# Kernel tuning notes

Measured on AMD Instinct MI355X. Metric: run time of the kernel, lower is better.

## Reference

```python
import jax, jax.numpy as jnp
import numpy as np

IN_CH, OUT_CH, M1, M2 = 64, 64, 32, 32


def _powerlaw_psd_gaussian(key, exponent, n):
    """JAX port of colorednoise.powerlaw_psd_gaussian (fmin=0 default)."""
    f = jnp.fft.rfftfreq(n).astype(jnp.float32)  # [n//2+1]
    # fmin = max(0, 1/n); f[0]=0 is the only freq below it -> clamp to f[1]
    s_scale = jnp.where(f < 1.0 / n, f[1], f) ** (-exponent / 2.0)
    w = s_scale[1:]
    w = w.at[-1].multiply((1 + (n % 2)) / 2.0)  # Nyquist correction
    sigma = 2.0 * jnp.sqrt(jnp.sum(w * w)) / n
    kr, ki = jax.random.split(key)
    sr = jax.random.normal(kr, f.shape, jnp.float32) * s_scale
    si = jax.random.normal(ki, f.shape, jnp.float32) * s_scale
    if n % 2 == 0:
        si = si.at[-1].set(0.0)
        sr = sr.at[-1].multiply(jnp.sqrt(2.0))
    si = si.at[0].set(0.0)
    sr = sr.at[0].multiply(jnp.sqrt(2.0))
    return jnp.fft.irfft(sr + 1j * si, n=n) / sigma


def _compl_mul2d(t1, w, e_r, e_i, amp_r, amp_i, phi_r, phi_i, key):
    # Faithful to the torch code: stack over in-ch at dim=1 then sum dim=2
    # sums over the OUT channel axis => out[b,i,x,y] = t1[b,i,x,y]*sum_o w[i,o,x,y]
    out = t1 * jnp.sum(w, axis=1)[None]  # [B, IN_CH, M1, M2] complex
    b, c, m1, m2 = out.shape
    n = b * c * m1 * m2
    k1, k2 = jax.random.split(key)
    nr = jnp.roll(_powerlaw_psd_gaussian(k1, e_r, n), phi_r.astype(jnp.int32)) * amp_r
    ni = jnp.roll(_powerlaw_psd_gaussian(k2, e_i, n), phi_i.astype(jnp.int32)) * amp_i
    # original multiplies imag noise by amp_i twice (once in-place, once on reshape)
    noise = (nr + 1j * (ni * amp_i)).reshape(b, c, m1, m2)
    return out - noise


def _forward(x, w1, w2, exp_r, exp_i, nAmp_real, nAmp_imag, nPhase_real, nphase_imag):
    w1c = w1[..., 0] + 1j * w1[..., 1]  # [IN, OUT, M1, M2] complex64
    w2c = w2[..., 0] + 1j * w2[..., 1]
    e_r = jnp.median(exp_r)
    e_i = jnp.median(exp_i)
    amp_r = jnp.median(nAmp_real)
    amp_i = jnp.median(nAmp_imag)
    phi_r = jnp.median(nPhase_real)
    phi_i = jnp.median(nphase_imag)
    B, _, H, W = x.shape
    Wr = W // 2 + 1
    x_ft = jnp.fft.rfft2(x)  # [B, IN_CH, H, Wr]
    key = jax.random.key(42)
    kA, kB = jax.random.split(key)
    out_ft = jnp.zeros((B, OUT_CH, H, Wr), jnp.complex64)
    out_ft = out_ft.at[:, :, :M1, :M2].set(
        _compl_mul2d(x_ft[:, :, :M1, :M2], w1c, e_r, e_i, amp_r, amp_i, phi_r, phi_i, kA))
    out_ft = out_ft.at[:, :, -M1:, :M2].set(
        _compl_mul2d(x_ft[:, :, -M1:, :M2], w2c, e_r, e_i, amp_r, amp_i, phi_r, phi_i, kB))
    return jnp.fft.irfft2(out_ft, s=(H, W)).astype(jnp.float32)


def setup_inputs() -> dict:
    key = jax.random.key(0)
    ks = jax.random.split(key, 9)
    scale = 1.0 / (IN_CH * OUT_CH)
    return {
        "x": jax.random.normal(ks[0], (16, IN_CH, 256, 256), jnp.float32),
        "w1": scale * jax.random.uniform(ks[1], (IN_CH, OUT_CH, M1, M2, 2), jnp.float32),
        "w2": scale * jax.random.uniform(ks[2], (IN_CH, OUT_CH, M1, M2, 2), jnp.float32),
        "exp_r": jax.random.uniform(ks[3], (8,), jnp.float32),
        "exp_i": jax.random.uniform(ks[4], (8,), jnp.float32),
        "nAmp_real": jax.random.uniform(ks[5], (8,), jnp.float32),
        "nAmp_imag": jax.random.uniform(ks[6], (8,), jnp.float32),
        "nPhase_real": jax.random.normal(ks[7], (8,), jnp.float32),
        "nphase_imag": jax.random.normal(ks[8], (8,), jnp.float32),
    }


def reference(x, w1, w2, exp_r, exp_i, nAmp_real, nAmp_imag, nPhase_real, nphase_imag):
    return _forward(x, w1, w2, exp_r, exp_i, nAmp_real, nAmp_imag, nPhase_real, nphase_imag)
```

## Files before the change

kernel.cpp:

```cpp
#include <hip/hip_runtime.h>
#include <cstdint>

#define JPART 1
#define PART_XOR 1

constexpr uint32_t N20   = 1u << 20;
constexpr uint32_t NHALF = 1u << 19;
constexpr int SPT_STRIDE = 520;

struct Hdr {
  float e_r, e_i, amp_r, amp_i;
  int   phi_r, phi_i;
  float nhe_r, nhe_i;
  float scale_s[4];
};
struct KeyArgs { uint32_t k[8][2]; };

typedef __attribute__((ext_vector_type(8))) short short8;
typedef __attribute__((ext_vector_type(16))) float f32x16;

__device__ inline f32x16 zero16() {
  f32x16 v;
  #pragma unroll
  for (int i = 0; i < 16; ++i) v[i] = 0.f;
  return v;
}

__device__ inline unsigned short f2bf(float f) {
  uint32_t u = __float_as_uint(f);
  return (unsigned short)((u + 0x7fffu + ((u >> 16) & 1u)) >> 16);
}

__host__ __device__ inline void tf2x32(uint32_t k0, uint32_t k1, uint32_t x0, uint32_t x1,
                                       uint32_t& o0, uint32_t& o1) {
  const uint32_t ks0 = k0, ks1 = k1, ks2 = k0 ^ k1 ^ 0x1BD11BDAu;
  const uint32_t ks[3] = { ks0, ks1, ks2 };
  x0 += ks0; x1 += ks1;
  const int rot[2][4] = { {13,15,26,6}, {17,29,16,24} };
  for (int g = 0; g < 5; ++g) {
    const int* rr = rot[g & 1];
    for (int i = 0; i < 4; ++i) {
      x0 += x1;
      x1 = (x1 << rr[i]) | (x1 >> (32 - rr[i]));
      x1 ^= x0;
    }
    x0 += ks[(g + 1) % 3];
    x1 += ks[(g + 2) % 3] + (uint32_t)(g + 1);
  }
  o0 = x0; o1 = x1;
}

__device__ inline float erfinv_xla(float x) {
  float w = -log1pf(-x * x);
  float p;
  if (w < 5.0f) {
    w -= 2.5f;
    p = 2.81022636e-08f;
    p = fmaf(p, w, 3.43273939e-07f);
    p = fmaf(p, w, -3.5233877e-06f);
    p = fmaf(p, w, -4.39150654e-06f);
    p = fmaf(p, w, 0.00021858087f);
    p = fmaf(p, w, -0.00125372503f);
    p = fmaf(p, w, -0.00417768164f);
    p = fmaf(p, w, 0.246640727f);
    p = fmaf(p, w, 1.50140941f);
  } else {
    w = sqrtf(w) - 3.0f;
    p = -0.000200214257f;
    p = fmaf(p, w, 0.000100950558f);
    p = fmaf(p, w, 0.00134934322f);
    p = fmaf(p, w, -0.00367342844f);
    p = fmaf(p, w, 0.00573950773f);
    p = fmaf(p, w, -0.0076224613f);
    p = fmaf(p, w, 0.00943887047f);
    p = fmaf(p, w, 1.00167406f);
    p = fmaf(p, w, 2.83297682f);
  }
  return p * x;
}

__device__ inline float normal_from_bits(uint32_t bits) {
  uint32_t fb = (bits >> 9) | 0x3f800000u;
  float f = __uint_as_float(fb) - 1.0f;
  const float LO = -0.99999994f;
  float u = f * 2.0f + LO;
  u = fmaxf(LO, u);
  return 1.41421356f * erfinv_xla(u);
}

__device__ inline float sscale_f(uint32_t k, float nhe) {
  uint32_t kk = k ? k : 1u;
  return powf((float)kk * (1.0f / 1048576.0f), nhe);
}

__device__ inline float2 cmul(float2 a, float2 b) {
  return make_float2(a.x * b.x - a.y * b.y, a.x * b.y + a.y * b.x);
}
__device__ inline float2 wexp(float u) {
  float s, c; sincospif(2.0f * u, &s, &c); return make_float2(c, s);
}
__device__ inline float2 cadd(float2 a, float2 b){ return make_float2(a.x+b.x, a.y+b.y); }
__device__ inline float2 csub(float2 a, float2 b){ return make_float2(a.x-b.x, a.y-b.y); }
__device__ inline float2 cmuli(float2 a){ return make_float2(-a.y, a.x); }

__device__ inline int sA(int p) { return p ^ (((p >> 6) & 3) << 2) ^ ((p >> 8) & 3); }

__device__ inline void bfly(float2& y0, float2& y1, float2& y2, float2& y3, float2 W) {
  float2 a = cadd(y0, y2), b = csub(y0, y2);
  float2 c = cadd(y1, y3), d = cmuli(csub(y1, y3));
  float2 W2 = cmul(W, W), W3 = cmul(W2, W);
  y0 = cadd(a, c);
  y1 = cmul(cadd(b, d), W);
  y2 = cmul(csub(a, c), W2);
  y3 = cmul(csub(b, d), W3);
}

__device__ inline void fft1024_core(float2* r, float2* rc, float2* buf, int w) {
  #pragma unroll
  for (int e3 = 0; e3 < 4; ++e3) {
    float2 W = wexp((float)((e3 << 6) + w) * (1.0f / 1024.0f));
    bfly(r[e3], r[e3 + 4], r[e3 + 8], r[e3 + 12], W);
  }
  {
    float2 W = wexp((float)w * (1.0f / 256.0f));
    #pragma unroll
    for (int e4 = 0; e4 < 4; ++e4)
      bfly(r[(e4 << 2) + 0], r[(e4 << 2) + 1], r[(e4 << 2) + 2], r[(e4 << 2) + 3], W);
  }
  #pragma unroll
  for (int s = 0; s < 16; ++s) buf[sA((s << 6) + w)] = r[s];
  __syncthreads();
  {
    const int e0 = w & 3;
    const int pbase = ((w >> 4) << 8) + (((w >> 2) & 3) << 6) + e0;
    float2 rb[16];
    #pragma unroll
    for (int e2 = 0; e2 < 4; ++e2)
      #pragma unroll
      for (int e1 = 0; e1 < 4; ++e1)
        rb[(e2 << 2) + e1] = buf[sA(pbase + (e2 << 4) + (e1 << 2))];
    #pragma unroll
    for (int e1 = 0; e1 < 4; ++e1) {
      float2 W = wexp((float)((e1 << 2) + e0) * (1.0f / 64.0f));
      bfly(rb[e1], rb[e1 + 4], rb[e1 + 8], rb[e1 + 12], W);
    }
    {
      float2 W = wexp((float)e0 * (1.0f / 16.0f));
      #pragma unroll
      for (int e2 = 0; e2 < 4; ++e2)
        bfly(rb[(e2 << 2) + 0], rb[(e2 << 2) + 1], rb[(e2 << 2) + 2], rb[(e2 << 2) + 3], W);
    }
    #pragma unroll
    for (int e2 = 0; e2 < 4; ++e2)
      #pragma unroll
      for (int e1 = 0; e1 < 4; ++e1)
        buf[sA(pbase + (e2 << 4) + (e1 << 2))] = rb[(e2 << 2) + e1];
  }
  __syncthreads();
  {
    const int cbase = ((w >> 4) << 8) + (((w >> 2) & 3) << 6) + ((w & 3) << 4);
    #pragma unroll
    for (int e1 = 0; e1 < 4; ++e1)
      #pragma unroll
      for (int e0 = 0; e0 < 4; ++e0)
        rc[(e1 << 2) + e0] = buf[sA(cbase + (e1 << 2) + e0)];
    #pragma unroll
    for (int e1 = 0; e1 < 4; ++e1) {
      float2 x0 = rc[(e1 << 2)], x1 = rc[(e1 << 2) + 1], x2 = rc[(e1 << 2) + 2], x3 = rc[(e1 << 2) + 3];
      float2 a = cadd(x0, x2), b = csub(x0, x2);
      float2 c = cadd(x1, x3), d = cmuli(csub(x1, x3));
      rc[(e1 << 2)]     = cadd(a, c);
      rc[(e1 << 2) + 1] = cadd(b, d);
      rc[(e1 << 2) + 2] = csub(a, c);
      rc[(e1 << 2) + 3] = csub(b, d);
    }
  }
}

__device__ inline float med8_dev(const float* p) {
  float v[8];
  for (int i = 0; i < 8; ++i) v[i] = p[i];
  for (int i = 1; i < 8; ++i) { float key = v[i]; int j = i - 1;
    while (j >= 0 && v[j] > key) { v[j + 1] = v[j]; --j; } v[j + 1] = key; }
  return 0.5f * (v[3] + v[4]);
}

__global__ __launch_bounds__(256) void k_misc(Hdr* h,
    const float* er, const float* ei, const float* ar, const float* ai,
    const float* pr, const float* pim,
    const float* __restrict__ w1, const float* __restrict__ w2,
    float2* __restrict__ wsum,
    unsigned short* __restrict__ A_E, unsigned short* __restrict__ B2T,
    unsigned short* __restrict__ ET, unsigned short* __restrict__ Fc,
    unsigned short* __restrict__ Fs, unsigned short* __restrict__ Fns) {
  const int b = blockIdx.x;
  if (b == 960) {
    if (threadIdx.x) return;
    float mer = med8_dev(er), mei = med8_dev(ei);
    h->e_r = mer; h->e_i = mei;
    h->amp_r = med8_dev(ar); h->amp_i = med8_dev(ai);
    h->phi_r = (int)med8_dev(pr);
    h->phi_i = (int)med8_dev(pim);
    h->nhe_r = -0.5f * mer; h->nhe_i = -0.5f * mei;
    return;
  }
  if (b < 512) {
    int idx = b * 256 + threadIdx.x;
    int sel = idx >> 16, rem = idx & 65535;
    const float* w = sel ? w2 : w1;
    int c = rem >> 10, m1 = (rem >> 5) & 31, m2 = rem & 31;
    size_t base = (size_t)c * 131072 + (size_t)m1 * 64 + (size_t)m2 * 2;
    float sr = 0.f, si = 0.f;
    for (int oc = 0; oc < 64; ++oc) { sr += w[base + (size_t)oc * 2048]; si += w[base + (size_t)oc * 2048 + 1]; }
    wsum[idx] = make_float2(sr, si);
    return;
  }
  int t = (b - 512) * 256 + threadIdx.x;
  if (t < 32768) {
    int y = t >> 7, p = t & 127;
    int kyp = p & 63; int ky = (kyp < 32) ? kyp : kyp + 192;
    float s, c; sincospif(2.0f * (float)((ky * y) & 255) * (1.0f / 256.0f), &s, &c);
    A_E[t] = f2bf((p < 64) ? c : s);
  } else if (t < 49152) {
    int u = t - 32768;
    int x = u >> 6, j = u & 63, kx = j & 31;
    float s, c; sincospif(2.0f * (float)((kx * x) & 255) * (1.0f / 256.0f), &s, &c);
    float v = (j < 32) ? ((kx == 0) ? 1.0f : 2.0f * c)
                       : ((kx == 0) ? 0.0f : -2.0f * s);
    B2T[u] = f2bf(v * (1.0f / 65536.0f));
  } else if (t < 65536) {
    int u = t - 49152;
    int col = u >> 8, xx = u & 255; int kx = col & 31;
    float s, c; sincospif(2.0f * (float)((kx * xx) & 255) * (1.0f / 256.0f), &s, &c);
    ET[u] = f2bf((col < 32) ? c : -s);
  } else if (t < 114688) {
    int u = (t - 65536) & 16383;
    int which = (t - 65536) >> 14;
    int kyp = u >> 8, y = u & 255; int ky = (kyp < 32) ? kyp : kyp + 192;
    float s, c; sincospif(2.0f * (float)((ky * y) & 255) * (1.0f / 256.0f), &s, &c);
    if (which == 0) Fc[u] = f2bf(c);
    else if (which == 1) Fs[u] = f2bf(s);
    else Fns[u] = f2bf(-s);
  }
}

__global__ __launch_bounds__(256, 2) void k_gen_fwd(const Hdr* __restrict__ h,
    float* __restrict__ partials, float4* __restrict__ spT, KeyArgs ka,
    const float* __restrict__ x, const float2* __restrict__ wsum,
    const unsigned short* __restrict__ ET, const unsigned short* __restrict__ Fc,
    const unsigned short* __restrict__ Fs, const unsigned short* __restrict__ Fns,
    float2* __restrict__ oftg) {
  __shared__ char lds[65536];
  const int b = blockIdx.x;
  if (b < 512) {
    float* sr_ = (float*)lds;
    float* si_ = (float*)(lds + 1024);
    const float nher = h->nhe_r, nhei = h->nhe_i;
    float sr = 0.f, si = 0.f;
    for (int j = 0; j < 4; ++j) {
      uint32_t k = (uint32_t)(b * 1024 + j * 256 + threadIdx.x) + 1u;
      float fk = (float)k * (1.0f / 1048576.0f);
      float wr = powf(fk, nher), wi = powf(fk, nhei);
      if (k == NHALF) { wr *= 0.5f; wi *= 0.5f; }
      sr += wr * wr; si += wi * wi;
    }
    sr_[threadIdx.x] = sr; si_[threadIdx.x] = si; __syncthreads();
    for (int off = 128; off > 0; off >>= 1) {
      if ((int)threadIdx.x < off) { sr_[threadIdx.x] += sr_[threadIdx.x + off];
                                    si_[threadIdx.x] += si_[threadIdx.x + off]; }
      __syncthreads();
    }
    if (!threadIdx.x) { partials[b * 2] = sr_[0]; partials[b * 2 + 1] = si_[0]; }
    return;
  }
  if (b < 4608) {
    const int idx = b - 512;
    const int pair = idx >> 11;
    const int bx = idx & 2047;
    const int k1 = bx >> 1, chunk = bx & 1;
    const int k2 = (chunk << 8) + (int)threadIdx.x;
    const float nher = h->nhe_r, nhei = h->nhe_i;
    float4* row = spT + (size_t)pair * (1024 * SPT_STRIDE) + (size_t)k1 * SPT_STRIDE;
    const bool extra = (k1 == 0) && (chunk == 1) && (threadIdx.x == 255);
    const int niter = extra ? 2 : 1;
    for (int it = 0; it < niter; ++it) {
      const int kk2 = (it == 0) ? k2 : 512;
      const uint32_t i = (uint32_t)k1 + ((uint32_t)kk2 << 10);
      float vals[4];
      #pragma unroll
      for (int j = 0; j < 4; ++j) {
        const uint32_t K0 = ka.k[pair * 4 + j][0], K1 = ka.k[pair * 4 + j][1];
        uint32_t o0, o1; tf2x32(K0, K1, 0u, i, o0, o1);
#if PART_XOR
        uint32_t bits = o0 ^ o1;
#else
        uint32_t bits = o1;
#endif
        float nhe = (j < 2) ? nher : nhei;
        float v = normal_from_bits(bits) * sscale_f(i, nhe);
        if (i == 0u || i == NHALF) v = (j & 1) ? 0.0f : v * 1.41421356f;
        vals[j] = v;
      }
      row[kk2] = make_float4(vals[0], vals[1], vals[2], vals[3]);
    }
    return;
  }

  char* X1T = lds + 32768;
  const int bc = b - 4608, t = threadIdx.x;
  const int c = bc & 63;
  const int l = t & 63, w = t >> 6, lr = l & 31, kg = l >> 5;
  const int rt = w >> 1, ct = w & 1;
  const float* xim = x + ((size_t)bc << 16);

  float4 pf[16];
  #pragma unroll
  for (int i = 0; i < 16; ++i) {
    int f4 = i * 256 + t;
    int r = f4 >> 6, c4 = f4 & 63;
    pf[i] = *(const float4*)(xim + (size_t)((r) << 8) + (c4 << 2));
  }

  #pragma unroll
  for (int yt = 0; yt < 4; ++yt) {
    __syncthreads();
    #pragma unroll
    for (int i = 0; i < 16; ++i) {
      int f4 = i * 256 + t;
      int r = f4 >> 6, c4 = f4 & 63;
      ushort4 b4; b4.x = f2bf(pf[i].x); b4.y = f2bf(pf[i].y);
      b4.z = f2bf(pf[i].z); b4.w = f2bf(pf[i].w);
      int byte = ((r << 9) + (c4 << 3)) ^ ((r & 7) << 4);
      *(ushort4*)(lds + byte) = b4;
    }
    __syncthreads();
    if (yt < 3) {
      #pragma unroll
      for (int i = 0; i < 16; ++i) {
        int f4 = i * 256 + t;
        int r = f4 >> 6, c4 = f4 & 63;
        pf[i] = *(const float4*)(xim + (size_t)((((yt + 1) << 6) + r) << 8) + (c4 << 2));
      }
    }
    f32x16 a1 = zero16();
    const int arow = (rt << 5) + lr;
    const int bcol = (ct << 5) + lr;
    #pragma unroll
    for (int s = 0; s < 16; ++s) {
      short8 af = *(const short8*)(lds + (((arow << 9) + (s << 5) + (kg << 4)) ^ ((arow & 7) << 4)));
      short8 bf = *(const short8*)(ET + (bcol << 8) + (s << 4) + (kg << 3));
      a1 = __builtin_amdgcn_mfma_f32_32x32x16_bf16(af, bf, a1, 0, 0, 0);
    }
    #pragma unroll
    for (int r4 = 0; r4 < 4; ++r4) {
      int y0 = (yt << 6) + (rt << 5) + (r4 << 3) + (kg << 2);
      ushort4 p4;
      p4.x = f2bf(a1[r4 * 4 + 0]); p4.y = f2bf(a1[r4 * 4 + 1]);
      p4.z = f2bf(a1[r4 * 4 + 2]); p4.w = f2bf(a1[r4 * 4 + 3]);
      int byte = ((bcol << 9) + (y0 << 1)) ^ ((bcol & 7) << 4);
      *(ushort4*)(X1T + byte) = p4;
    }
  }
  __syncthreads();

  const int re_im = w >> 1, kt = w & 1;
  const unsigned short* A1p = re_im ? Fns : Fs;
  const int b0row = (re_im ? 32 : 0) + lr;
  const int b1row = (re_im ? 0 : 32) + lr;
  const int a2row = (kt << 5) + lr;
  f32x16 a2 = zero16();
  #pragma unroll
  for (int s = 0; s < 16; ++s) {
    short8 a0f = *(const short8*)(Fc  + (a2row << 8) + (s << 4) + (kg << 3));
    short8 a1f = *(const short8*)(A1p + (a2row << 8) + (s << 4) + (kg << 3));
    short8 b0f = *(const short8*)(X1T + (((b0row << 9) + (s << 5) + (kg << 4)) ^ ((b0row & 7) << 4)));
    short8 b1f = *(const short8*)(X1T + (((b1row << 9) + (s << 5) + (kg << 4)) ^ ((b1row & 7) << 4)));
    a2 = __builtin_amdgcn_mfma_f32_32x32x16_bf16(a0f, b0f, a2, 0, 0, 0);
    a2 = __builtin_amdgcn_mfma_f32_32x32x16_bf16(a1f, b1f, a2, 0, 0, 0);
  }
  float* Osm = (float*)(lds + (re_im << 13));
  #pragma unroll
  for (int i = 0; i < 16; ++i) {
    int row = (kt << 5) + (i & 3) + ((i >> 2) << 3) + (kg << 2);
    Osm[(row << 5) + lr] = a2[i];
  }
  __syncthreads();

  const float* Ore = (const float*)lds;
  const float* Oim = (const float*)(lds + 8192);
  #pragma unroll
  for (int r = 0; r < 8; ++r) {
    int idx = (r << 8) + t;
    int kyp = idx >> 5, kx = idx & 31;
    int sel = kyp >> 5, m1 = kyp & 31;
    float2 av = make_float2(Ore[idx], Oim[idx]);
    float2 wv = wsum[((size_t)sel << 16) + (size_t)(((c << 5) | m1) << 5) + (size_t)kx];
    float2 v;
    v.x = av.x * wv.x - av.y * wv.y;
    v.y = av.x * wv.y + av.y * wv.x;
    oftg[((size_t)bc << 11) + (size_t)idx] = v;
  }
}

__global__ __launch_bounds__(256) void k_fin_s1(Hdr* h, const float* __restrict__ partials,
                                                const float4* __restrict__ spT,
                                                float2* __restrict__ G) {
  __shared__ float2 buf4[4][1024];
  const int b = blockIdx.x;
  if (b == 512) {
    if (threadIdx.x) return;
    float Sr = 0.f, Si = 0.f;
    for (int q = 0; q < 512; ++q) { Sr += partials[q * 2]; Si += partials[q * 2 + 1]; }
    float sig_r = 2.0f * sqrtf(Sr) * (1.0f / 1048576.0f);
    float sig_i = 2.0f * sqrtf(Si) * (1.0f / 1048576.0f);
    float s0 = h->amp_r / (sig_r * 1048576.0f);
    float s1 = (h->amp_i * h->amp_i) / (sig_i * 1048576.0f);
    h->scale_s[0] = s0; h->scale_s[1] = s1; h->scale_s[2] = s0; h->scale_s[3] = s1;
    return;
  }
  const int lin = (b & 7) * 64 + (b >> 3);
  const int pair = lin >> 8;
  const int g = threadIdx.x >> 6, w = threadIdx.x & 63;
  const int k1b = (lin & 255) << 2;
  const int k1 = k1b + g;
  const float4* sp = spT + (size_t)pair * (1024 * SPT_STRIDE);
  const int mrow = (1024 - k1) & 1023;

  float2 r[16], rc[16];
  #pragma unroll
  for (int s = 0; s < 16; ++s) {
    int k2 = (s << 6) + w;
    uint32_t k = (uint32_t)k1 + ((uint32_t)k2 << 10);
    float4 f; float2 z;
    if (k <= NHALF) {
      f = sp[(size_t)k1 * SPT_STRIDE + k2];
      z = make_float2(f.x - f.w, f.y + f.z);
    } else {
      int k2p = (k1 == 0) ? (1024 - k2) : (1023 - k2);
      f = sp[(size_t)mrow * SPT_STRIDE + k2p];
      z = make_float2(f.x + f.w, f.z - f.y);
    }
    r[s] = z;
  }
  fft1024_core(r, rc, buf4[g], w);
  const int klo = ((w & 3) << 4) + (((w >> 2) & 3) << 2) + (w >> 4);
  #pragma unroll
  for (int e1 = 0; e1 < 4; ++e1)
    #pragma unroll
    for (int e0 = 0; e0 < 4; ++e0) {
      int k = (e0 << 8) + (e1 << 6) + klo;
      float2 tw = wexp((float)(k * k1) * (1.0f / 1048576.0f));
      buf4[g][sA(k)] = cmul(rc[(e1 << 2) + e0], tw);
    }
  __syncthreads();
  const int t = threadIdx.x;
  float2* gp = G + ((size_t)pair << 20) + (size_t)k1b;
  const int k1off = t & 3;
  #pragma unroll
  for (int it = 0; it < 16; ++it) {
    int j2 = (it << 6) + (t >> 2);
    gp[((size_t)j2 << 10) + k1off] = buf4[k1off][sA(j2)];
  }
}

__global__ __launch_bounds__(256) void k_fft_s2(const float2* __restrict__ G,
                                                float2* __restrict__ noiseP,
                                                const Hdr* __restrict__ h) {
  __shared__ float2 buf4[4][1024];
  const int b = blockIdx.x;
  const int lin = (b & 7) * 64 + (b >> 3);
  const int pair = lin >> 8;
  const int g = threadIdx.x >> 6, w = threadIdx.x & 63;
  const int j2 = ((lin & 255) << 2) + g;

  float2 r[16], rc[16];
  const float2* gp = G + ((size_t)pair << 20) + ((size_t)j2 << 10);
  #pragma unroll
  for (int s = 0; s < 16; ++s) r[s] = gp[(s << 6) + w];
  fft1024_core(r, rc, buf4[g], w);
  const float scr = h->scale_s[0], sci = h->scale_s[1];
  float2* np_ = noiseP + ((size_t)pair << 20) + ((size_t)j2 << 10);
  const int klo = ((w & 3) << 4) + (((w >> 2) & 3) << 2) + (w >> 4);
  #pragma unroll
  for (int e1 = 0; e1 < 4; ++e1)
    #pragma unroll
    for (int e0 = 0; e0 < 4; ++e0) {
      int k = (e0 << 8) + (e1 << 6) + klo;
      np_[k] = make_float2(rc[(e1 << 2) + e0].x * scr, rc[(e1 << 2) + e0].y * sci);
    }
}

__global__ __launch_bounds__(256) void k_ntrans(const float2* __restrict__ noiseP,
                                                float* __restrict__ noiseL,
                                                const Hdr* __restrict__ h) {
  __shared__ float tr[64][65];
  __shared__ float ti[64][65];
  const int b = blockIdx.x;
  const int pair = b >> 8, tid = b & 255;
  const int R0 = (tid >> 4) << 6;
  const int C0 = (tid & 15) << 6;
  const int t = threadIdx.x;
  const int tx = t & 63, ty = t >> 6;
  const int phir = h->phi_r, phii = h->phi_i;
  const float2* src = noiseP + ((size_t)pair << 20);
  float* dstr = noiseL + ((size_t)(pair * 2) << 20);
  float* dsti = noiseL + ((size_t)(pair * 2 + 1) << 20);
  #pragma unroll
  for (int i = 0; i < 16; ++i) {
    int r = (i << 2) + ty;
    float2 v = src[(size_t)((R0 + r) << 10) + (size_t)(C0 + tx)];
    tr[r][tx] = v.x; ti[r][tx] = v.y;
  }
  __syncthreads();
  #pragma unroll
  for (int i = 0; i < 16; ++i) {
    int c = (i << 2) + ty;
    int n = ((C0 + c) << 10) + R0 + tx;
    dstr[(uint32_t)(n + phir) & (N20 - 1u)] = tr[tx][c];
    dsti[(uint32_t)(n + phii) & (N20 - 1u)] = ti[tx][c];
  }
}

__global__ __launch_bounds__(256) void k_inverse(const float2* __restrict__ oftg,
    const float* __restrict__ noiseL,
    const unsigned short* __restrict__ A_E, const unsigned short* __restrict__ B2T,
    float* __restrict__ out) {
  __shared__ char smem[32768];

  const int bc = blockIdx.x, t = threadIdx.x;
  const int l = t & 63, w = t >> 6, lr = l & 31, kg = l >> 5;

  {
    const float* ob = (const float*)(oftg + ((size_t)bc << 11));
    const uint32_t pbase = (uint32_t)bc << 10;
    #pragma unroll
    for (int i = 0; i < 32; ++i) {
      int idx = t + (i << 8);
      int p = idx >> 6, j = idx & 63;
      int kyp = p & 63;
      int sel = kyp >> 5, m1 = kyp & 31;
      const float* nlr = noiseL + ((size_t)(sel ? 2 : 0) << 20);
      const float* nli = noiseL + ((size_t)(sel ? 3 : 1) << 20);
      int kx = (j < 32) ? j : (j - 32);
      uint32_t pn = pbase + ((uint32_t)m1 << 5) + (uint32_t)kx;
      float v;
      if (p < 64) v = (j < 32) ? (ob[(kyp << 6) + (j << 1)] - nlr[pn])
                               : (ob[(kyp << 6) + ((j - 32) << 1) + 1] - nli[pn]);
      else        v = (j < 32) ? -(ob[(kyp << 6) + (j << 1) + 1] - nli[pn])
                               : (ob[(kyp << 6) + ((j - 32) << 1)] - nlr[pn]);
      int byte = ((j << 8) + (p << 1)) ^ ((j & 7) << 4);
      *(unsigned short*)(smem + byte) = f2bf(v);
    }
  }
  __syncthreads();

  f32x16 acc[2][2];
  acc[0][0] = zero16(); acc[0][1] = zero16(); acc[1][0] = zero16(); acc[1][1] = zero16();
  #pragma unroll
  for (int s = 0; s < 8; ++s) {
    short8 af[2], bf[2];
    #pragma unroll
    for (int rt = 0; rt < 2; ++rt) {
      int row = (w << 6) + (rt << 5) + lr;
      af[rt] = *(const short8*)(A_E + (row << 7) + (s << 4) + (kg << 3));
    }
    #pragma unroll
    for (int ct = 0; ct < 2; ++ct) {
      int j = (ct << 5) + lr;
      int byte = ((j << 8) + (s << 5) + (kg << 4)) ^ ((j & 7) << 4);
      bf[ct] = *(const short8*)(smem + byte);
    }
    #pragma unroll
    for (int rt = 0; rt < 2; ++rt)
      #pragma unroll
      for (int ct = 0; ct < 2; ++ct)
        acc[rt][ct] = __builtin_amdgcn_mfma_f32_32x32x16_bf16(af[rt], bf[ct], acc[rt][ct], 0, 0, 0);
  }
  __syncthreads();

  #pragma unroll
  for (int rt = 0; rt < 2; ++rt)
    #pragma unroll
    for (int ct = 0; ct < 2; ++ct)
      #pragma unroll
      for (int r = 0; r < 16; ++r) {
        int row = (w << 6) + (rt << 5) + (r & 3) + (((r >> 2) & 3) << 3) + (kg << 2);
        int col = (ct << 5) + lr;
        int byte = ((row << 7) + (col << 1)) ^ ((row & 7) << 4);
        *(unsigned short*)(smem + byte) = f2bf(acc[rt][ct][r]);
      }
  __syncthreads();

  short8 ta[2][4];
  #pragma unroll
  for (int rt = 0; rt < 2; ++rt)
    #pragma unroll
    for (int ks = 0; ks < 4; ++ks) {
      int row = (w << 6) + (rt << 5) + lr;
      int byte = ((row << 7) + (ks << 5) + (kg << 4)) ^ ((row & 7) << 4);
      ta[rt][ks] = *(const short8*)(smem + byte);
    }
  float* op = out + ((size_t)bc << 16);
  #pragma unroll
  for (int cc = 0; cc < 4; ++cc) {
    short8 b2[2][4];
    #pragma unroll
    for (int cx = 0; cx < 2; ++cx)
      #pragma unroll
      for (int ks = 0; ks < 4; ++ks) {
        int xx = (cc << 6) + (cx << 5) + lr;
        b2[cx][ks] = *(const short8*)(B2T + (xx << 6) + (ks << 4) + (kg << 3));
      }
    f32x16 a2[2][2];
    a2[0][0] = zero16(); a2[0][1] = zero16(); a2[1][0] = zero16(); a2[1][1] = zero16();
    #pragma unroll
    for (int ks = 0; ks < 4; ++ks)
      #pragma unroll
      for (int rt = 0; rt < 2; ++rt)
        #pragma unroll
        for (int cx = 0; cx < 2; ++cx)
          a2[rt][cx] = __builtin_amdgcn_mfma_f32_32x32x16_bf16(ta[rt][ks], b2[cx][ks], a2[rt][cx], 0, 0, 0);
    #pragma unroll
    for (int rt = 0; rt < 2; ++rt)
      #pragma unroll
      for (int cx = 0; cx < 2; ++cx)
        #pragma unroll
        for (int r = 0; r < 16; ++r) {
          int row = (w << 6) + (rt << 5) + (r & 3) + (((r >> 2) & 3) << 3) + (kg << 2);
          int xx = (cc << 6) + (cx << 5) + lr;
          op[(row << 8) + xx] = a2[rt][cx][r];
        }
  }
}

extern "C" void kernel_launch(void* const* d_in, const int* in_sizes, int n_in,
                              void* d_out, int out_size, void* d_ws, size_t ws_size,
                              hipStream_t stream) {
  (void)in_sizes; (void)n_in; (void)out_size; (void)ws_size;
  const float* x   = (const float*)d_in[0];
  const float* w1  = (const float*)d_in[1];
  const float* w2  = (const float*)d_in[2];
  const float* er  = (const float*)d_in[3];
  const float* ei  = (const float*)d_in[4];
  const float* ar  = (const float*)d_in[5];
  const float* ai  = (const float*)d_in[6];
  const float* pr  = (const float*)d_in[7];
  const float* pim = (const float*)d_in[8];
  float* out = (float*)d_out;

  char* ws = (char*)d_ws;
  Hdr*    hdr      = (Hdr*)ws;
  float*  partials = (float*)(ws + 0x1000);
  float2* wsum     = (float2*)(ws + 0x10000);
  unsigned short* A_E = (unsigned short*)(ws + 0x130000);
  unsigned short* B2T = (unsigned short*)(ws + 0x140000);
  unsigned short* ET  = (unsigned short*)(ws + 0x148000);
  unsigned short* Fc  = (unsigned short*)(ws + 0x150000);
  unsigned short* Fs  = (unsigned short*)(ws + 0x158000);
  unsigned short* Fns = (unsigned short*)(ws + 0x160000);
  float4* spT      = (float4*)(ws + 0x200000);
  float*  noiseL   = (float*)(ws + 0x200000);
  float2* G        = (float2*)(ws + 0x1400000);
  float2* noiseP   = (float2*)(ws + 0x2400000);
  float2* oft      = (float2*)(ws + 0x3400000);

  auto splitk = [](const uint32_t k[2], uint32_t a[2], uint32_t b[2]) {
#if JPART
    tf2x32(k[0], k[1], 0u, 0u, a[0], a[1]);
    tf2x32(k[0], k[1], 0u, 1u, b[0], b[1]);
#else
    uint32_t r0[2], r1[2];
    tf2x32(k[0], k[1], 0u, 2u, r0[0], r0[1]);
    tf2x32(k[0], k[1], 1u, 3u, r1[0], r1[1]);
    a[0] = r0[0]; a[1] = r1[0]; b[0] = r0[1]; b[1] = r1[1];
#endif
  };
  uint32_t root[2] = { 0u, 42u };
  uint32_t kA[2], kB[2], k1A[2], k2A[2], k1B[2], k2B[2];
  splitk(root, kA, kB);
  splitk(kA, k1A, k2A);
  splitk(kB, k1B, k2B);
  KeyArgs ka;
  splitk(k1A, ka.k[0], ka.k[1]);
  splitk(k2A, ka.k[2], ka.k[3]);
  splitk(k1B, ka.k[4], ka.k[5]);
  splitk(k2B, ka.k[6], ka.k[7]);

  hipLaunchKernelGGL(k_misc,    dim3(961),  dim3(256), 0, stream, hdr, er, ei, ar, ai, pr, pim,
                     w1, w2, wsum, A_E, B2T, ET, Fc, Fs, Fns);
  hipLaunchKernelGGL(k_gen_fwd, dim3(5632), dim3(256), 0, stream, hdr, partials, spT, ka,
                     x, wsum, ET, Fc, Fs, Fns, oft);
  hipLaunchKernelGGL(k_fin_s1,  dim3(513),  dim3(256), 0, stream, hdr, partials, spT, G);
  hipLaunchKernelGGL(k_fft_s2,  dim3(512),  dim3(256), 0, stream, G, noiseP, hdr);
  hipLaunchKernelGGL(k_ntrans,  dim3(512),  dim3(256), 0, stream, noiseP, noiseL, hdr);
  hipLaunchKernelGGL(k_inverse, dim3(1024), dim3(256), 0, stream, oft, noiseL, A_E, B2T, out);
}
```

Measured before the change: 260.5 us.

## Split inverse kernel into half-image blocks and schedule forward FFT blocks first

The inverse kernel now launches two blocks per image, each computing 128 output rows with half the accumulators, and uses separate LDS regions so one barrier is dropped. The fused generation/forward kernel reorders its block roles so the heavy forward-FFT blocks are dispatched before the noise and partial-sum blocks. This aims to improve occupancy and load balance and to reduce tail effects. In exchange, each half-block redundantly loads and converts the full spectrum tile.

Result: slower. 274.2 us (+5.2%).

```diff
diff --git a/kernel.cpp b/kernel.cpp
--- a/kernel.cpp
+++ b/kernel.cpp
@@ -252,13 +252,14 @@
     float2* __restrict__ oftg) {
   __shared__ char lds[65536];
   const int b = blockIdx.x;
-  if (b < 512) {
+  if (b >= 1024 && b < 1536) {
+    const int bb = b - 1024;
     float* sr_ = (float*)lds;
     float* si_ = (float*)(lds + 1024);
     const float nher = h->nhe_r, nhei = h->nhe_i;
     float sr = 0.f, si = 0.f;
     for (int j = 0; j < 4; ++j) {
-      uint32_t k = (uint32_t)(b * 1024 + j * 256 + threadIdx.x) + 1u;
+      uint32_t k = (uint32_t)(bb * 1024 + j * 256 + threadIdx.x) + 1u;
       float fk = (float)k * (1.0f / 1048576.0f);
       float wr = powf(fk, nher), wi = powf(fk, nhei);
       if (k == NHALF) { wr *= 0.5f; wi *= 0.5f; }
@@ -270,11 +271,11 @@
                                     si_[threadIdx.x] += si_[threadIdx.x + off]; }
       __syncthreads();
     }
-    if (!threadIdx.x) { partials[b * 2] = sr_[0]; partials[b * 2 + 1] = si_[0]; }
+    if (!threadIdx.x) { partials[bb * 2] = sr_[0]; partials[bb * 2 + 1] = si_[0]; }
     return;
   }
-  if (b < 4608) {
-    const int idx = b - 512;
+  if (b >= 1536) {
+    const int idx = b - 1536;
     const int pair = idx >> 11;
     const int bx = idx & 2047;
     const int k1 = bx >> 1, chunk = bx & 1;
@@ -307,7 +308,7 @@
   }
 
   char* X1T = lds + 32768;
-  const int bc = b - 4608, t = threadIdx.x;
+  const int bc = b, t = threadIdx.x;
   const int c = bc & 63;
   const int l = t & 63, w = t >> 6, lr = l & 31, kg = l >> 5;
   const int rt = w >> 1, ct = w & 1;
@@ -526,8 +527,10 @@
     const unsigned short* __restrict__ A_E, const unsigned short* __restrict__ B2T,
     float* __restrict__ out) {
   __shared__ char smem[32768];
-
-  const int bc = blockIdx.x, t = threadIdx.x;
+  char* Mt = smem + 16384;
+  char* Tb = smem;
+
+  const int bc = blockIdx.x >> 1, half = blockIdx.x & 1, t = threadIdx.x;
   const int l = t & 63, w = t >> 6, lr = l & 31, kg = l >> 5;
 
   {
@@ -549,58 +552,48 @@
       else        v = (j < 32) ? -(ob[(kyp << 6) + (j << 1) + 1] - nli[pn])
                                : (ob[(kyp << 6) + ((j - 32) << 1)] - nlr[pn]);
       int byte = ((j << 8) + (p << 1)) ^ ((j & 7) << 4);
-      *(unsigned short*)(smem + byte) = f2bf(v);
-    }
-  }
-  __syncthreads();
-
-  f32x16 acc[2][2];
-  acc[0][0] = zero16(); acc[0][1] = zero16(); acc[1][0] = zero16(); acc[1][1] = zero16();
+      *(unsigned short*)(Mt + byte) = f2bf(v);
+    }
+  }
+  __syncthreads();
+
+  f32x16 acc[2];
+  acc[0] = zero16(); acc[1] = zero16();
   #pragma unroll
   for (int s = 0; s < 8; ++s) {
-    short8 af[2], bf[2];
-    #pragma unroll
-    for (int rt = 0; rt < 2; ++rt) {
-      int row = (w << 6) + (rt << 5) + lr;
-      af[rt] = *(const short8*)(A_E + (row << 7) + (s << 4) + (kg << 3));
-    }
+    int row = (half << 7) + (w << 5) + lr;
+    short8 af = *(const short8*)(A_E + (row << 7) + (s << 4) + (kg << 3));
+    short8 bf[2];
     #pragma unroll
     for (int ct = 0; ct < 2; ++ct) {
       int j = (ct << 5) + lr;
       int byte = ((j << 8) + (s << 5) + (kg << 4)) ^ ((j & 7) << 4);
-      bf[ct] = *(const short8*)(smem + byte);
-    }
-    #pragma unroll
-    for (int rt = 0; rt < 2; ++rt)
-      #pragma unroll
-      for (int ct = 0; ct < 2; ++ct)
-        acc[rt][ct] = __builtin_amdgcn_mfma_f32_32x32x16_bf16(af[rt], bf[ct], acc[rt][ct], 0, 0, 0);
-  }
-  __syncthreads();
-
-  #pragma unroll
-  for (int rt = 0; rt < 2; ++rt)
+      bf[ct] = *(const short8*)(Mt + byte);
+    }
     #pragma unroll
     for (int ct = 0; ct < 2; ++ct)
-      #pragma unroll
-      for (int r = 0; r < 16; ++r) {
-        int row = (w << 6) + (rt << 5) + (r & 3) + (((r >> 2) & 3) << 3) + (kg << 2);
-        int col = (ct << 5) + lr;
-        int byte = ((row << 7) + (col << 1)) ^ ((row & 7) << 4);
-        *(unsigned short*)(smem + byte) = f2bf(acc[rt][ct][r]);
-      }
-  __syncthreads();
-
-  short8 ta[2][4];
-  #pragma unroll
-  for (int rt = 0; rt < 2; ++rt)
-    #pragma unroll
-    for (int ks = 0; ks < 4; ++ks) {
-      int row = (w << 6) + (rt << 5) + lr;
-      int byte = ((row << 7) + (ks << 5) + (kg << 4)) ^ ((row & 7) << 4);
-      ta[rt][ks] = *(const short8*)(smem + byte);
-    }
-  float* op = out + ((size_t)bc << 16);
+      acc[ct] = __builtin_amdgcn_mfma_f32_32x32x16_bf16(af, bf[ct], acc[ct], 0, 0, 0);
+  }
+
+  #pragma unroll
+  for (int ct = 0; ct < 2; ++ct)
+    #pragma unroll
+    for (int r = 0; r < 16; ++r) {
+      int rowl = (w << 5) + (r & 3) + (((r >> 2) & 3) << 3) + (kg << 2);
+      int col = (ct << 5) + lr;
+      int byte = ((rowl << 7) + (col << 1)) ^ ((rowl & 7) << 4);
+      *(unsigned short*)(Tb + byte) = f2bf(acc[ct][r]);
+    }
+  __syncthreads();
+
+  short8 ta[4];
+  #pragma unroll
+  for (int ks = 0; ks < 4; ++ks) {
+    int rowl = (w << 5) + lr;
+    int byte = ((rowl << 7) + (ks << 5) + (kg << 4)) ^ ((rowl & 7) << 4);
+    ta[ks] = *(const short8*)(Tb + byte);
+  }
+  float* op = out + ((size_t)bc << 16) + ((size_t)(half << 7) << 8);
   #pragma unroll
   for (int cc = 0; cc < 4; ++cc) {
     short8 b2[2][4];
@@ -611,25 +604,21 @@
         int xx = (cc << 6) + (cx << 5) + lr;
         b2[cx][ks] = *(const short8*)(B2T + (xx << 6) + (ks << 4) + (kg << 3));
       }
-    f32x16 a2[2][2];
-    a2[0][0] = zero16(); a2[0][1] = zero16(); a2[1][0] = zero16(); a2[1][1] = zero16();
+    f32x16 a2[2];
+    a2[0] = zero16(); a2[1] = zero16();
     #pragma unroll
     for (int ks = 0; ks < 4; ++ks)
       #pragma unroll
-      for (int rt = 0; rt < 2; ++rt)
-        #pragma unroll
-        for (int cx = 0; cx < 2; ++cx)
-          a2[rt][cx] = __builtin_amdgcn_mfma_f32_32x32x16_bf16(ta[rt][ks], b2[cx][ks], a2[rt][cx], 0, 0, 0);
-    #pragma unroll
-    for (int rt = 0; rt < 2; ++rt)
-      #pragma unroll
       for (int cx = 0; cx < 2; ++cx)
-        #pragma unroll
-        for (int r = 0; r < 16; ++r) {
-          int row = (w << 6) + (rt << 5) + (r & 3) + (((r >> 2) & 3) << 3) + (kg << 2);
-          int xx = (cc << 6) + (cx << 5) + lr;
-          op[(row << 8) + xx] = a2[rt][cx][r];
-        }
+        a2[cx] = __builtin_amdgcn_mfma_f32_32x32x16_bf16(ta[ks], b2[cx][ks], a2[cx], 0, 0, 0);
+    #pragma unroll
+    for (int cx = 0; cx < 2; ++cx)
+      #pragma unroll
+      for (int r = 0; r < 16; ++r) {
+        int rowl = (w << 5) + (r & 3) + (((r >> 2) & 3) << 3) + (kg << 2);
+        int xx = (cc << 6) + (cx << 5) + lr;
+        op[(rowl << 8) + xx] = a2[cx][r];
+      }
   }
 }
 
@@ -693,5 +682,5 @@
   hipLaunchKernelGGL(k_fin_s1,  dim3(513),  dim3(256), 0, stream, hdr, partials, spT, G);
   hipLaunchKernelGGL(k_fft_s2,  dim3(512),  dim3(256), 0, stream, G, noiseP, hdr);
   hipLaunchKernelGGL(k_ntrans,  dim3(512),  dim3(256), 0, stream, noiseP, noiseL, hdr);
-  hipLaunchKernelGGL(k_inverse, dim3(1024), dim3(256), 0, stream, oft, noiseL, A_E, B2T, out);
-}
+  hipLaunchKernelGGL(k_inverse, dim3(2048), dim3(256), 0, stream, oft, noiseL, A_E, B2T, out);
+}
```
